# Optimization experiments

Measured on AMD Instinct MI355X. Metric: run time of the kernel, lower is better.

## Reference

```python
import jax, jax.numpy as jnp
from jax import lax
import numpy as np

N, E, G, CPG = 4096, 16, 14, 8  # wafers, experts, groups (wafer sub-arrays), channels per group
C = G * CPG  # 112


def setup_inputs() -> dict:
    key = jax.random.key(0)
    ks = jax.random.split(key, 9)
    s = 0.05
    x = jax.random.normal(ks[0], (N, G, 8, 8), jnp.float32)
    keys = jax.random.randint(ks[1], (N,), 0, E)
    # hexagonal wafer conv mask (buffer in the torch module); corners zeroed
    conv_mask = jnp.array([[1.0, 1.0, 0.0], [1.0, 1.0, 1.0], [0.0, 1.0, 1.0]], jnp.float32)
    enc_conv_w = jax.random.normal(ks[2], (E, C, 1, 3, 3), jnp.float32) * s
    enc_dense_w = jax.random.normal(ks[3], (E, G, 8, 128), jnp.float32) * s
    enc_dense_b = jax.random.normal(ks[4], (E, G, 8), jnp.float32) * s
    dec_dense_w = jax.random.normal(ks[5], (E, G, 128, 8), jnp.float32) * s
    dec_dense_b = jax.random.normal(ks[6], (E, G, 128), jnp.float32) * s
    dec_tconv_w = jax.random.normal(ks[7], (E, C, 1, 3, 3), jnp.float32) * s
    dec_tconv_b = jax.random.normal(ks[8], (E, G), jnp.float32) * s
    return dict(x=x, keys=keys, conv_mask=conv_mask,
                enc_conv_w=enc_conv_w, enc_dense_w=enc_dense_w, enc_dense_b=enc_dense_b,
                dec_dense_w=dec_dense_w, dec_dense_b=dec_dense_b,
                dec_tconv_w=dec_tconv_w, dec_tconv_b=dec_tconv_b)


def reference(x, keys, conv_mask, enc_conv_w, enc_dense_w, enc_dense_b,
              dec_dense_w, dec_dense_b, dec_tconv_w, dec_tconv_b):
    n = x.shape[0]
    dn = ('NCHW', 'OIHW', 'NCHW')

    # ---- encoder: masked grouped conv (bias=False) ----
    wc = enc_conv_w[keys] * conv_mask  # [N,112,1,3,3]; mask broadcasts over spatial taps

    def enc_conv(xi, wi):
        return lax.conv_general_dilated(xi[None], wi, (1, 1), 'SAME',
                                        feature_group_count=G, dimension_numbers=dn)[0]

    h = jax.nn.relu(jax.vmap(enc_conv)(x, wc))           # [N,112,8,8]
    h = h.reshape(n, C, 4, 2, 4, 2).max(axis=(3, 5))     # MaxPool2d(2) -> [N,112,4,4]
    feat = h.reshape(n, G, CPG * 16)                      # [N,14,128] (group-major, matches torch view)
    z = jax.nn.relu(jnp.einsum('ngof,ngf->ngo', enc_dense_w[keys], feat) + enc_dense_b[keys])  # [N,14,8]

    # ---- decoder ----
    y = jax.nn.relu(jnp.einsum('ngfo,ngo->ngf', dec_dense_w[keys], z) + dec_dense_b[keys])  # [N,14,128]
    y = y.reshape(n, C, 4, 4)

    # ConvTranspose2d(112,14,3,stride=2,pad=1,outpad=1,groups=14) as a dilated forward conv
    # with spatially flipped kernels: per group, 8 in -> 1 out.
    wt = jnp.flip(dec_tconv_w[keys].reshape(n, G, CPG, 3, 3), axis=(-2, -1))  # [N,14,8,3,3] OIHW
    bt = dec_tconv_b[keys]  # [N,14]

    def dec_tconv(yi, wi, bi):
        o = lax.conv_general_dilated(yi[None], wi, (1, 1), ((1, 2), (1, 2)),
                                     lhs_dilation=(2, 2), feature_group_count=G,
                                     dimension_numbers=dn)[0]
        return o + bi[:, None, None]

    out = jax.vmap(dec_tconv)(y, wt, bt)  # [N,14,8,8]
    return jax.nn.relu(out)
```

## Files before the change

kernel.cpp:

```cpp
#include <hip/hip_runtime.h>
#include <hip/hip_fp16.h>

#define NG 14
#define NE 16
#define NW 32
#define YW 148

typedef __fp16 h2 __attribute__((ext_vector_type(2)));
typedef __fp16 h4 __attribute__((ext_vector_type(4)));
typedef __fp16 h8 __attribute__((ext_vector_type(8)));

__device__ __forceinline__ float hdot4(h4 a, h4 b, float c) {
    const h2 a0 = __builtin_shufflevector(a, a, 0, 1);
    const h2 a1 = __builtin_shufflevector(a, a, 2, 3);
    const h2 b0 = __builtin_shufflevector(b, b, 0, 1);
    const h2 b1 = __builtin_shufflevector(b, b, 2, 3);
    return __builtin_amdgcn_fdot2(a1, b1, __builtin_amdgcn_fdot2(a0, b0, c, false), false);
}

__global__ __launch_bounds__(1024) void bin_kernel(const int* __restrict__ keys, int N,
                                                   int NBW, int* __restrict__ sorted) {
    __shared__ int hist[NE], offs[NE], cur[NE];
    __shared__ int runTot;
    const int t = threadIdx.x;
    if (t < NE) { hist[t] = 0; cur[t] = 0; }
    __syncthreads();
    for (int i = t; i < N; i += 1024) atomicAdd(&hist[keys[i]], 1);
    __syncthreads();
    if (t == 0) {
        int run = 0;
        for (int e = 0; e < NE; ++e) { offs[e] = run; run += (hist[e] + NW - 1) & ~(NW - 1); }
        runTot = run;
    }
    __syncthreads();
    for (int i = t; i < N; i += 1024) {
        const int e = keys[i];
        sorted[offs[e] + atomicAdd(&cur[e], 1)] = i;
    }
    {
        const int e = t >> 6, l = t & 63;
        const int cnt = hist[e];
        const int padded = (cnt + NW - 1) & ~(NW - 1);
        if (l < padded - cnt) sorted[offs[e] + cnt + l] = -1;
    }
    for (int i = runTot + t; i < NBW; i += 1024) sorted[i] = -1;
}

#define XEL(R,C) (((R) < 0 || (R) > 7 || (C) < 0 || (C) > 7) ? 0.f : xv[(R)&7][(C)&7])

__global__ __launch_bounds__(256, 4) void ae_main(
    const float* __restrict__ x,
    const int*   __restrict__ keys,
    const float* __restrict__ conv_mask,
    const float* __restrict__ enc_conv_w,
    const float* __restrict__ enc_dense_w,
    const float* __restrict__ enc_dense_b,
    const float* __restrict__ dec_dense_w,
    const float* __restrict__ dec_dense_b,
    const float* __restrict__ dec_tconv_w,
    const float* __restrict__ dec_tconv_b,
    const int*   __restrict__ sorted,
    float* __restrict__ out)
{
    const int t = threadIdx.x;
    const int chunk = blockIdx.x / NG;
    const int g = blockIdx.x - chunk * NG;

    __shared__ __attribute__((aligned(16))) __half yt[NW * YW];
    __shared__ __attribute__((aligned(16))) h2 ews2[640];
    __shared__ __attribute__((aligned(16))) h2 dws2[512];
    __shared__ __attribute__((aligned(16))) h2 wtr2[48];
    __shared__ __attribute__((aligned(16))) float wcs[72];
    __shared__ float dbs[128];
    __shared__ float ebs[8];

    const int* chunkIds = sorted + chunk * NW;
    const int i0 = chunkIds[0];
    if (i0 < 0) return;
    const int k = keys[i0];

    const int w = t >> 3, ch = t & 7;
    const int idw = chunkIds[w];
    const int idr = (idw < 0) ? i0 : idw;

    const float* xg = x + (size_t)idr * 896 + g * 64;
    float xv[8][8];
    #pragma unroll
    for (int r = 0; r < 8; ++r) {
        const float4 a = *(const float4*)(xg + r * 8);
        const float4 b = *(const float4*)(xg + r * 8 + 4);
        xv[r][0]=a.x; xv[r][1]=a.y; xv[r][2]=a.z; xv[r][3]=a.w;
        xv[r][4]=b.x; xv[r][5]=b.y; xv[r][6]=b.z; xv[r][7]=b.w;
    }

    const size_t wg1024 = (size_t)(k * NG + g) * 1024;
    {
        const float4 w4 = *(const float4*)(enc_dense_w + wg1024 + 4 * t);
        const int o = t >> 5, c2 = (t >> 2) & 7, pr = t & 3;
        const int base = (pr * 8 + c2) * 20 + o * 2;
        ews2[base]     = __builtin_amdgcn_cvt_pkrtz(w4.x, w4.y);
        ews2[base + 1] = __builtin_amdgcn_cvt_pkrtz(w4.z, w4.w);
    }
    if (t < 128) {
        const float4 a = *(const float4*)(dec_dense_w + wg1024 + 8 * t);
        const float4 b = *(const float4*)(dec_dense_w + wg1024 + 8 * t + 4);
        const int c2 = t >> 4, p = t & 15;
        h2* dst = &dws2[(p * 8 + c2) * 4];
        dst[0] = __builtin_amdgcn_cvt_pkrtz(a.x, a.y);
        dst[1] = __builtin_amdgcn_cvt_pkrtz(a.z, a.w);
        dst[2] = __builtin_amdgcn_cvt_pkrtz(b.x, b.y);
        dst[3] = __builtin_amdgcn_cvt_pkrtz(b.z, b.w);
    } else if (t < 200) {
        const int i = t - 128, c2 = i / 9, tap = i - c2 * 9;
        wcs[tap * 8 + c2] = enc_conv_w[(size_t)k * 1008 + (g * 8 + c2) * 9 + tap] * conv_mask[tap];
    } else if (t < 208) {
        ebs[t - 200] = enc_dense_b[(size_t)k * 112 + g * 8 + (t - 200)];
    } else if (t < 256) {
        const int i = t - 208, tap = i >> 2, j = i & 3;
        h2 v = (h2)(__fp16)0.f;
        if (tap < 9) {
            const float wa = dec_tconv_w[(size_t)k * 1008 + (g * 8 + 2*j) * 9 + tap];
            const float wb = dec_tconv_w[(size_t)k * 1008 + (g * 8 + 2*j + 1) * 9 + tap];
            v = __builtin_amdgcn_cvt_pkrtz(wa, wb);
        }
        wtr2[tap * 4 + j] = v;
    }
    if (t < 128) {
        dbs[(t & 15) * 8 + (t >> 4)] = dec_dense_b[(size_t)k * 1792 + g * 128 + t];
    }
    __syncthreads();

    const float w0 = wcs[0*8+ch], w1 = wcs[1*8+ch], w3 = wcs[3*8+ch], w4 = wcs[4*8+ch],
                w5 = wcs[5*8+ch], w7 = wcs[7*8+ch], w8 = wcs[8*8+ch];
    float part[8] = {0.f,0.f,0.f,0.f,0.f,0.f,0.f,0.f};
    #pragma unroll
    for (int pr = 0; pr < 4; ++pr) {
        float res[4];
        #pragma unroll
        for (int pc = 0; pc < 4; ++pc) {
            float mx = 0.f;
            #pragma unroll
            for (int rl = 0; rl < 2; ++rl) {
                #pragma unroll
                for (int cl = 0; cl < 2; ++cl) {
                    const int ir = 2*pr + rl, jc = 2*pc + cl;
                    const float s = w0*XEL(ir-1,jc-1) + w1*XEL(ir-1,jc)
                                  + w3*XEL(ir,jc-1)  + w4*XEL(ir,jc) + w5*XEL(ir,jc+1)
                                  + w7*XEL(ir+1,jc)  + w8*XEL(ir+1,jc+1);
                    mx = fmaxf(mx, s);
                }
            }
            res[pc] = mx;
        }
        const h2 ra = __builtin_amdgcn_cvt_pkrtz(res[0], res[1]);
        const h2 rb = __builtin_amdgcn_cvt_pkrtz(res[2], res[3]);
        const h2* eb2 = &ews2[(pr * 8 + ch) * 20];
        #pragma unroll
        for (int q = 0; q < 4; ++q) {
            const h8 v = *(const h8*)(eb2 + q * 4);
            const h2 a0 = __builtin_shufflevector(v, v, 0, 1);
            const h2 a1 = __builtin_shufflevector(v, v, 2, 3);
            const h2 b0 = __builtin_shufflevector(v, v, 4, 5);
            const h2 b1 = __builtin_shufflevector(v, v, 6, 7);
            part[2*q]   = __builtin_amdgcn_fdot2(rb, a1, __builtin_amdgcn_fdot2(ra, a0, part[2*q],   false), false);
            part[2*q+1] = __builtin_amdgcn_fdot2(rb, b1, __builtin_amdgcn_fdot2(ra, b0, part[2*q+1], false), false);
        }
    }

    float z[8];
    #pragma unroll
    for (int o = 0; o < 8; ++o) {
        float v = part[o];
        v += __shfl_xor(v, 1);
        v += __shfl_xor(v, 2);
        v += __shfl_xor(v, 4);
        z[o] = fmaxf(v + ebs[o], 0.f);
    }
    const h2 z01 = __builtin_amdgcn_cvt_pkrtz(z[0], z[1]);
    const h2 z23 = __builtin_amdgcn_cvt_pkrtz(z[2], z[3]);
    const h2 z45 = __builtin_amdgcn_cvt_pkrtz(z[4], z[5]);
    const h2 z67 = __builtin_amdgcn_cvt_pkrtz(z[6], z[7]);

    __half* yw_ = yt + w * YW;
    #pragma unroll
    for (int p = 0; p < 16; ++p) {
        const h8 v = *(const h8*)(&dws2[(p * 8 + ch) * 4]);
        const h2 v0 = __builtin_shufflevector(v, v, 0, 1);
        const h2 v1 = __builtin_shufflevector(v, v, 2, 3);
        const h2 v2 = __builtin_shufflevector(v, v, 4, 5);
        const h2 v3 = __builtin_shufflevector(v, v, 6, 7);
        float acc = dbs[p * 8 + ch];
        acc = __builtin_amdgcn_fdot2(z01, v0, acc, false);
        acc = __builtin_amdgcn_fdot2(z23, v1, acc, false);
        acc = __builtin_amdgcn_fdot2(z45, v2, acc, false);
        acc = __builtin_amdgcn_fdot2(z67, v3, acc, false);
        yw_[(p >> 2) * 36 + (p & 3) * 8 + ch] = __float2half(fmaxf(acc, 0.f));
    }
    __syncthreads();

    const int oi = ch;
    int iA, rA, iB, rB;
    if ((oi & 1) == 0) { iA = oi >> 1; rA = 3; iB = 0; rB = 9; }
    else { iA = (oi - 1) >> 1; rA = 6;
           if (oi < 7) { iB = (oi + 1) >> 1; rB = 0; } else { iB = 0; rB = 9; } }
    const float bias = dec_tconv_b[k * NG + g];
    const __fp16* ywh = (const __fp16*)(yt) + w * YW;
    float acc[8] = {0.f,0.f,0.f,0.f,0.f,0.f,0.f,0.f};
    #pragma unroll
    for (int hc = 0; hc < 2; ++hc) {
        const h4 wA0 = *(const h4*)(wtr2 + (rA + 0) * 4 + hc * 2);
        const h4 wA1 = *(const h4*)(wtr2 + (rA + 1) * 4 + hc * 2);
        const h4 wA2 = *(const h4*)(wtr2 + (rA + 2) * 4 + hc * 2);
        const h4 wB0 = *(const h4*)(wtr2 + (rB + 0) * 4 + hc * 2);
        const h4 wB1 = *(const h4*)(wtr2 + (rB + 1) * 4 + hc * 2);
        const h4 wB2 = *(const h4*)(wtr2 + (rB + 2) * 4 + hc * 2);
        h4 yA[4], yB[4];
        #pragma unroll
        for (int j = 0; j < 4; ++j) {
            yA[j] = *(const h4*)(ywh + iA * 36 + j * 8 + hc * 4);
            yB[j] = *(const h4*)(ywh + iB * 36 + j * 8 + hc * 4);
        }
        acc[0] = hdot4(wB1, yB[0], hdot4(wA1, yA[0], acc[0]));
        acc[1] = hdot4(wB0, yB[1], hdot4(wB2, yB[0],
                 hdot4(wA0, yA[1], hdot4(wA2, yA[0], acc[1]))));
        acc[2] = hdot4(wB1, yB[1], hdot4(wA1, yA[1], acc[2]));
        acc[3] = hdot4(wB0, yB[2], hdot4(wB2, yB[1],
                 hdot4(wA0, yA[2], hdot4(wA2, yA[1], acc[3]))));
        acc[4] = hdot4(wB1, yB[2], hdot4(wA1, yA[2], acc[4]));
        acc[5] = hdot4(wB0, yB[3], hdot4(wB2, yB[2],
                 hdot4(wA0, yA[3], hdot4(wA2, yA[2], acc[5]))));
        acc[6] = hdot4(wB1, yB[3], hdot4(wA1, yA[3], acc[6]));
        acc[7] = hdot4(wB2, yB[3], hdot4(wA2, yA[3], acc[7]));
    }
    if (idw >= 0) {
        float* og = out + (size_t)idw * 896 + g * 64 + oi * 8;
        *(float4*)(og)     = make_float4(fmaxf(acc[0]+bias,0.f), fmaxf(acc[1]+bias,0.f),
                                         fmaxf(acc[2]+bias,0.f), fmaxf(acc[3]+bias,0.f));
        *(float4*)(og + 4) = make_float4(fmaxf(acc[4]+bias,0.f), fmaxf(acc[5]+bias,0.f),
                                         fmaxf(acc[6]+bias,0.f), fmaxf(acc[7]+bias,0.f));
    }
}

extern "C" void kernel_launch(void* const* d_in, const int* in_sizes, int n_in,
                              void* d_out, int out_size, void* d_ws, size_t ws_size,
                              hipStream_t stream) {
    const float* x            = (const float*)d_in[0];
    const int*   keys         = (const int*)d_in[1];
    const float* conv_mask    = (const float*)d_in[2];
    const float* enc_conv_w   = (const float*)d_in[3];
    const float* enc_dense_w  = (const float*)d_in[4];
    const float* enc_dense_b  = (const float*)d_in[5];
    const float* dec_dense_w  = (const float*)d_in[6];
    const float* dec_dense_b  = (const float*)d_in[7];
    const float* dec_tconv_w  = (const float*)d_in[8];
    const float* dec_tconv_b  = (const float*)d_in[9];
    float* out = (float*)d_out;

    const int N = in_sizes[0] / (NG * 64);
    const int CHUNKS = (N + NE * (NW - 1)) / NW + 1;
    int* sorted = (int*)d_ws;

    bin_kernel<<<1, 1024, 0, stream>>>(keys, N, CHUNKS * NW, sorted);
    ae_main<<<CHUNKS * NG, 256, 0, stream>>>(
        x, keys, conv_mask, enc_conv_w, enc_dense_w, enc_dense_b,
        dec_dense_w, dec_dense_b, dec_tconv_w, dec_tconv_b, sorted, out);
}
```

Measured before the change: 27.95 us.

## Fuse expert binning into main kernel, removing separate single-block sort launch

```diff
diff --git a/kernel.cpp b/kernel.cpp
--- a/kernel.cpp
+++ b/kernel.cpp
@@ -16,34 +16,6 @@
     const h2 b0 = __builtin_shufflevector(b, b, 0, 1);
     const h2 b1 = __builtin_shufflevector(b, b, 2, 3);
     return __builtin_amdgcn_fdot2(a1, b1, __builtin_amdgcn_fdot2(a0, b0, c, false), false);
-}
-
-__global__ __launch_bounds__(1024) void bin_kernel(const int* __restrict__ keys, int N,
-                                                   int NBW, int* __restrict__ sorted) {
-    __shared__ int hist[NE], offs[NE], cur[NE];
-    __shared__ int runTot;
-    const int t = threadIdx.x;
-    if (t < NE) { hist[t] = 0; cur[t] = 0; }
-    __syncthreads();
-    for (int i = t; i < N; i += 1024) atomicAdd(&hist[keys[i]], 1);
-    __syncthreads();
-    if (t == 0) {
-        int run = 0;
-        for (int e = 0; e < NE; ++e) { offs[e] = run; run += (hist[e] + NW - 1) & ~(NW - 1); }
-        runTot = run;
-    }
-    __syncthreads();
-    for (int i = t; i < N; i += 1024) {
-        const int e = keys[i];
-        sorted[offs[e] + atomicAdd(&cur[e], 1)] = i;
-    }
-    {
-        const int e = t >> 6, l = t & 63;
-        const int cnt = hist[e];
-        const int padded = (cnt + NW - 1) & ~(NW - 1);
-        if (l < padded - cnt) sorted[offs[e] + cnt + l] = -1;
-    }
-    for (int i = runTot + t; i < NBW; i += 1024) sorted[i] = -1;
 }
 
 #define XEL(R,C) (((R) < 0 || (R) > 7 || (C) < 0 || (C) > 7) ? 0.f : xv[(R)&7][(C)&7])
@@ -59,12 +31,13 @@
     const float* __restrict__ dec_dense_b,
     const float* __restrict__ dec_tconv_w,
     const float* __restrict__ dec_tconv_b,
-    const int*   __restrict__ sorted,
+    const int    N,
     float* __restrict__ out)
 {
     const int t = threadIdx.x;
     const int chunk = blockIdx.x / NG;
     const int g = blockIdx.x - chunk * NG;
+    const int lane = t & 63, wid = t >> 6;
 
     __shared__ __attribute__((aligned(16))) __half yt[NW * YW];
     __shared__ __attribute__((aligned(16))) h2 ews2[640];
@@ -73,25 +46,31 @@
     __shared__ __attribute__((aligned(16))) float wcs[72];
     __shared__ float dbs[128];
     __shared__ float ebs[8];
-
-    const int* chunkIds = sorted + chunk * NW;
-    const int i0 = chunkIds[0];
-    if (i0 < 0) return;
-    const int k = keys[i0];
-
-    const int w = t >> 3, ch = t & 7;
-    const int idw = chunkIds[w];
-    const int idr = (idw < 0) ? i0 : idw;
-
-    const float* xg = x + (size_t)idr * 896 + g * 64;
-    float xv[8][8];
-    #pragma unroll
-    for (int r = 0; r < 8; ++r) {
-        const float4 a = *(const float4*)(xg + r * 8);
-        const float4 b = *(const float4*)(xg + r * 8 + 4);
-        xv[r][0]=a.x; xv[r][1]=a.y; xv[r][2]=a.z; xv[r][3]=a.w;
-        xv[r][4]=b.x; xv[r][5]=b.y; xv[r][6]=b.z; xv[r][7]=b.w;
-    }
+    __shared__ int hist[NE];
+    __shared__ unsigned long long segmask[64];
+    __shared__ int segpre[64];
+    __shared__ int sids[NW];
+    __shared__ int ebx[2];
+
+    if (t < NE) hist[t] = 0;
+    if (t < NW) sids[t] = -1;
+    __syncthreads();
+    for (int i = t; i < N; i += 256) atomicAdd(&hist[keys[i]], 1);
+    __syncthreads();
+    if (t == 0) {
+        int run = 0, e = -1, lo = 0;
+        const int base = chunk * NW;
+        for (int ee = 0; ee < NE; ++ee) {
+            const int padded = (hist[ee] + NW - 1) & ~(NW - 1);
+            if (e < 0 && base >= run && base < run + padded) { e = ee; lo = base - run; }
+            run += padded;
+        }
+        ebx[0] = e; ebx[1] = lo;
+    }
+    __syncthreads();
+    const int k = ebx[0];
+    const int lo = ebx[1];
+    if (k < 0) return;
 
     const size_t wg1024 = (size_t)(k * NG + g) * 1024;
     {
@@ -114,7 +93,7 @@
         const int i = t - 128, c2 = i / 9, tap = i - c2 * 9;
         wcs[tap * 8 + c2] = enc_conv_w[(size_t)k * 1008 + (g * 8 + c2) * 9 + tap] * conv_mask[tap];
     } else if (t < 208) {
-        ebs[t - 200] = enc_dense_b[(size_t)k * 112 + g * 8 + (t - 200)];
+        ebs[t - 200] = enc_dense_b[(size_t)k * 112 + g * 8 + (t - 208 + 8)];
     } else if (t < 256) {
         const int i = t - 208, tap = i >> 2, j = i & 3;
         h2 v = (h2)(__fp16)0.f;
@@ -128,7 +107,52 @@
     if (t < 128) {
         dbs[(t & 15) * 8 + (t >> 4)] = dec_dense_b[(size_t)k * 1792 + g * 128 + t];
     }
-    __syncthreads();
+
+    for (int it = 0; it * 256 < N; ++it) {
+        const int i = it * 256 + t;
+        const unsigned long long bm = __ballot(i < N && keys[i] == k);
+        if (lane == 0) segmask[it * 4 + wid] = bm;
+    }
+    __syncthreads();
+    if (t < 64) {
+        const int nseg = ((N + 255) >> 8) * 4;
+        int c = 0;
+        if (t < nseg) c = __popcll(segmask[t]);
+        int inc = c;
+        #pragma unroll
+        for (int off = 1; off < 64; off <<= 1) {
+            const int v = __shfl_up(inc, off);
+            if (lane >= off) inc += v;
+        }
+        segpre[t] = inc - c;
+    }
+    __syncthreads();
+    {
+        const unsigned long long ltmask = (1ULL << lane) - 1ULL;
+        for (int it = 0; it * 256 < N; ++it) {
+            const int i = it * 256 + t;
+            if (i < N && keys[i] == k) {
+                const int s = segpre[it * 4 + wid]
+                            + __popcll(segmask[it * 4 + wid] & ltmask) - lo;
+                if (s >= 0 && s < NW) sids[s] = i;
+            }
+        }
+    }
+    __syncthreads();
+
+    const int w = t >> 3, ch = t & 7;
+    const int idw = sids[w];
+    const int idr = (idw < 0) ? sids[0] : idw;
+
+    const float* xg = x + (size_t)idr * 896 + g * 64;
+    float xv[8][8];
+    #pragma unroll
+    for (int r = 0; r < 8; ++r) {
+        const float4 a = *(const float4*)(xg + r * 8);
+        const float4 b = *(const float4*)(xg + r * 8 + 4);
+        xv[r][0]=a.x; xv[r][1]=a.y; xv[r][2]=a.z; xv[r][3]=a.w;
+        xv[r][4]=b.x; xv[r][5]=b.y; xv[r][6]=b.z; xv[r][7]=b.w;
+    }
 
     const float w0 = wcs[0*8+ch], w1 = wcs[1*8+ch], w3 = wcs[3*8+ch], w4 = wcs[4*8+ch],
                 w5 = wcs[5*8+ch], w7 = wcs[7*8+ch], w8 = wcs[8*8+ch];
@@ -258,10 +282,8 @@
 
     const int N = in_sizes[0] / (NG * 64);
     const int CHUNKS = (N + NE * (NW - 1)) / NW + 1;
-    int* sorted = (int*)d_ws;
-
-    bin_kernel<<<1, 1024, 0, stream>>>(keys, N, CHUNKS * NW, sorted);
+
     ae_main<<<CHUNKS * NG, 256, 0, stream>>>(
         x, keys, conv_mask, enc_conv_w, enc_dense_w, enc_dense_b,
-        dec_dense_w, dec_dense_b, dec_tconv_w, dec_tconv_b, sorted, out);
+        dec_dense_w, dec_dense_b, dec_tconv_w, dec_tconv_b, N, out);
 }
```

Measured after the change: 38.42 us. +37.5%, slower.
